# Performance work log

Measured on AMD Instinct MI355X. Metric: run time of the kernel, lower is better.

## Reference

```python
import jax, jax.numpy as jnp
import numpy as np

SCALE_FACTOR = 4.0
DROPOUT_P = 0.5
DROPOUT_KEY = jax.random.key(42)  # fixed key: torch dropout is stochastic; we fix RNG for reproducibility


def setup_inputs() -> dict:
    key = jax.random.key(0)
    k1, k2 = jax.random.split(key)
    x1 = jax.random.normal(k1, (4096, 1024), dtype=jnp.float32)
    x2 = jax.random.normal(k2, (4096, 1024), dtype=jnp.float32)
    return {"x1": x1, "x2": x2}


def reference(x1, x2):
    # scores: [M, N] = x1 @ x2^T, scaled
    scores = jnp.matmul(x1, x2.T) * SCALE_FACTOR
    # F.softmax with no dim on 2-D input -> softmax over dim 1 (keys)
    attn = jax.nn.softmax(scores, axis=-1)
    # dropout p=0.5, train mode (inverted dropout: scale kept units by 1/(1-p))
    keep = jax.random.bernoulli(DROPOUT_KEY, 1.0 - DROPOUT_P, attn.shape)
    attn = jnp.where(keep, attn / (1.0 - DROPOUT_P), 0.0).astype(attn.dtype)
    # output: [M, D] = attn @ x2 (x2 reused as values)
    return jnp.matmul(attn, x2)
```

## Files before the change

### kernel.cpp

```cpp
#include <hip/hip_runtime.h>

typedef unsigned short u16;
typedef unsigned int   u32;
typedef __attribute__((ext_vector_type(4))) float f32x4;
typedef __attribute__((ext_vector_type(8))) short bf16x8;
typedef __attribute__((ext_vector_type(8))) unsigned short u16x8;
typedef __attribute__((ext_vector_type(4))) unsigned short u16x4;

#define MROWS 4096
#define DDIM  1024

__device__ __forceinline__ u16 f2bf(float f) {
  u32 u = __float_as_uint(f);
  return (u16)((u + 0x7FFFu + ((u >> 16) & 1u)) >> 16);
}
__device__ __forceinline__ float bf2f(u16 h) { return __uint_as_float(((u32)h) << 16); }

__device__ __forceinline__ u32 rotl32(u32 x, int r) { return (x << r) | (x >> (32 - r)); }
__device__ __forceinline__ u32 threefry_bits(u32 n) {
  const u32 K0 = 0u, K1 = 42u, K2 = 0x1BD11BDAu ^ 0u ^ 42u;
  u32 x0 = K0;
  u32 x1 = n + K1;
#define TF4(a,b,c,d) \
  x0 += x1; x1 = rotl32(x1, a); x1 ^= x0; \
  x0 += x1; x1 = rotl32(x1, b); x1 ^= x0; \
  x0 += x1; x1 = rotl32(x1, c); x1 ^= x0; \
  x0 += x1; x1 = rotl32(x1, d); x1 ^= x0;
  TF4(13,15,26,6);  x0 += K1; x1 += K2 + 1u;
  TF4(17,29,16,24); x0 += K2; x1 += K0 + 2u;
  TF4(13,15,26,6);  x0 += K0; x1 += K1 + 3u;
  TF4(17,29,16,24); x0 += K1; x1 += K2 + 4u;
  TF4(13,15,26,6);  x0 += K2; x1 += K0 + 5u;
#undef TF4
  return x0 ^ x1;
}

__global__ __launch_bounds__(256)
void expandA(const float4* __restrict__ x, u16* __restrict__ out) {
  int t = blockIdx.x * 256 + threadIdx.x;
  float4 v0 = x[(size_t)t * 2], v1 = x[(size_t)t * 2 + 1];
  float vv[8] = {v0.x*4.f, v0.y*4.f, v0.z*4.f, v0.w*4.f,
                 v1.x*4.f, v1.y*4.f, v1.z*4.f, v1.w*4.f};
  u16 o[24];
#pragma unroll
  for (int j = 0; j < 8; ++j) {
    u16 h = f2bf(vv[j]);
    u16 l = f2bf(vv[j] - bf2f(h));
    o[3*j] = h; o[3*j+1] = h; o[3*j+2] = l;
  }
  u16x8* dst = (u16x8*)(out + (size_t)t * 24);
#pragma unroll
  for (int q = 0; q < 3; ++q) {
    u16x8 wv;
#pragma unroll
    for (int j = 0; j < 8; ++j) wv[j] = o[q*8+j];
    dst[q] = wv;
  }
}

__global__ __launch_bounds__(256)
void castB_transpose(const float* __restrict__ x2, u16* __restrict__ XB,
                     u16* __restrict__ VT) {
  __shared__ float tile[64][65];
  int tid = threadIdx.x;
  int dt = blockIdx.x;
  int kt = blockIdx.y;
#pragma unroll
  for (int it = 0; it < 16; ++it) {
    int lin = it * 256 + tid;
    int r = lin >> 6, c = lin & 63;
    tile[r][c] = x2[(size_t)(kt*64 + r) * DDIM + dt*64 + c];
  }
  __syncthreads();
#pragma unroll
  for (int itr = 0; itr < 2; ++itr) {
    int r  = (tid >> 3) + itr * 32;
    int c0 = (tid & 7) * 8;
    u16 o[24];
#pragma unroll
    for (int j = 0; j < 8; ++j) {
      float v = tile[r][c0 + j];
      u16 h = f2bf(v);
      u16 l = f2bf(v - bf2f(h));
      o[3*j] = h; o[3*j+1] = l; o[3*j+2] = h;
    }
    u16x8* dst = (u16x8*)(XB + (size_t)(kt*64 + r) * 3072 + (size_t)(dt*64 + c0) * 3);
#pragma unroll
    for (int q = 0; q < 3; ++q) {
      u16x8 wv;
#pragma unroll
      for (int j = 0; j < 8; ++j) wv[j] = o[q*8+j];
      dst[q] = wv;
    }
  }
#pragma unroll
  for (int it = 0; it < 16; ++it) {
    int lin = it * 256 + tid;
    int dr = lin >> 6, kc = lin & 63;
    VT[(size_t)(dt*64 + dr) * MROWS + kt*64 + kc] = f2bf(tile[kc][dr]);
  }
}

__device__ __forceinline__ void gload16(const u16* g, u16* l) {
  __builtin_amdgcn_global_load_lds(
      (const __attribute__((address_space(1))) void*)g,
      (__attribute__((address_space(3))) void*)l, 16, 0, 0);
}

#define BARRIER() do { asm volatile("" ::: "memory"); __builtin_amdgcn_s_barrier(); \
                       asm volatile("" ::: "memory"); } while (0)
#define VMCNT(N)  asm volatile("s_waitcnt vmcnt(" #N ")" ::: "memory")
#define PRIO1()   __builtin_amdgcn_s_setprio(1)
#define PRIO0()   __builtin_amdgcn_s_setprio(0)

__device__ __forceinline__ void mma_quad(f32x4 (&acc)[8][4], const bf16x8 (&aF)[4][2],
                                         const bf16x8 (&bF)[2][2], int MH, int NH) {
#pragma unroll
  for (int kx = 0; kx < 2; ++kx)
#pragma unroll
    for (int m = 0; m < 4; ++m)
#pragma unroll
      for (int n = 0; n < 2; ++n)
        acc[MH*4+m][NH*2+n] = __builtin_amdgcn_mfma_f32_16x16x32_bf16(
            aF[m][kx], bF[n][kx], acc[MH*4+m][NH*2+n], 0, 0, 0);
}

template <bool OUT16, bool REMAP>
__global__ __launch_bounds__(512, 2)
void gemm256(const u16* __restrict__ A, const u16* __restrict__ Bt, void* __restrict__ Cv,
             int M, int N, int K, int ntpc) {
  __shared__ u16 smem[65536];
  const int tid = threadIdx.x;
  const int lane = tid & 63;
  const int w = tid >> 6;
  const int wr = w >> 2;
  const int wc = w & 3;
  const int fr = lane & 15;
  const int hi = lane >> 4;

  int bxi, byi;
  if (REMAP) {
    const int id0 = blockIdx.y * gridDim.x + blockIdx.x;
    const int c = id0 & 7, j = id0 >> 3;
    bxi = j >> 1;
    byi = c * 2 + (j & 1);
  } else {
    bxi = blockIdx.x; byi = blockIdx.y;
  }

  const long bm = (long)byi * 256;
  const long bn = (long)bxi * 256;
  const size_t kcol0 = (size_t)blockIdx.z * ntpc * 64;

  const int srow = tid >> 3;
  const int scol = (((tid & 7) ^ (srow & 7)) << 3);
  const u16* Abase = A  + (size_t)(bm + srow) * K + kcol0 + scol;
  const u16* Bbase = Bt + (size_t)(bn + srow) * K + kcol0 + scol;

  const int csw0 = ((hi)     ^ (fr & 7)) << 3;
  const int csw1 = ((4 + hi) ^ (fr & 7)) << 3;
  const int arow = (wr*16 + fr) * 64;
  const int brow = (wc*16 + fr) * 64;

#define RD_A(dst, D, H) do { \
    const u16* _b0 = smem + ((D)*2+(H))*8192 + arow + csw0; \
    const u16* _b1 = smem + ((D)*2+(H))*8192 + arow + csw1; \
    dst[0][0] = *(const bf16x8*)(_b0);        dst[0][1] = *(const bf16x8*)(_b1); \
    dst[1][0] = *(const bf16x8*)(_b0 + 2048); dst[1][1] = *(const bf16x8*)(_b1 + 2048); \
    dst[2][0] = *(const bf16x8*)(_b0 + 4096); dst[2][1] = *(const bf16x8*)(_b1 + 4096); \
    dst[3][0] = *(const bf16x8*)(_b0 + 6144); dst[3][1] = *(const bf16x8*)(_b1 + 6144); } while (0)
#define RD_B(dst, D, H) do { \
    const u16* _b0 = smem + 32768 + ((D)*2+(H))*8192 + brow + csw0; \
    const u16* _b1 = smem + 32768 + ((D)*2+(H))*8192 + brow + csw1; \
    dst[0][0] = *(const bf16x8*)(_b0);        dst[0][1] = *(const bf16x8*)(_b1); \
    dst[1][0] = *(const bf16x8*)(_b0 + 4096); dst[1][1] = *(const bf16x8*)(_b1 + 4096); } while (0)

  f32x4 acc[8][4];
#pragma unroll
  for (int m = 0; m < 8; ++m)
#pragma unroll
    for (int n = 0; n < 4; ++n) acc[m][n] = (f32x4){0.f, 0.f, 0.f, 0.f};
  bf16x8 a0[4][2], a1[4][2], b0[2][2], b1[2][2];

#define STAGE_A(TAU,H,D) do { \
    const u16* _s = Abase + (size_t)(H)*128*K + (size_t)(TAU)*64; \
    u16* _d = smem + ((D)*2+(H))*8192 + tid*8; \
    gload16(_s, _d); gload16(_s + (size_t)64*K, _d + 4096); } while (0)
#define STAGE_B(TAU,H,D) do { \
    const u16* _s = Bbase + (size_t)(H)*128*K + (size_t)(TAU)*64; \
    u16* _d = smem + 32768 + ((D)*2+(H))*8192 + tid*8; \
    gload16(_s, _d); gload16(_s + (size_t)64*K, _d + 4096); } while (0)

  STAGE_A(0,0,0); STAGE_B(0,0,0);
  VMCNT(0); BARRIER();
  RD_A(a0, 0, 0); RD_B(b0, 0, 0);
  STAGE_B(0,1,0);
  STAGE_A(0,1,0);
  STAGE_A(1,0,1); STAGE_B(1,0,1);
  STAGE_B(1,1,1);
  STAGE_A(1,1,1);
  VMCNT(10); BARRIER();

  const int nt = ntpc;
  for (int T = 0; T < nt; T += 2) {
    const int t2 = (T + 2 < nt) ? T + 2 : nt - 1;
    const int t3 = (T + 3 < nt) ? T + 3 : nt - 1;

    RD_B(b1, 0, 1);
    PRIO1(); mma_quad(acc, a0, b0, 0, 0); PRIO0();
    VMCNT(8);  BARRIER();
    RD_A(a1, 0, 1);
    STAGE_A(t2, 0, 0); STAGE_B(t2, 0, 0);
    PRIO1(); mma_quad(acc, a0, b1, 0, 1); PRIO0();
    BARRIER();
    STAGE_B(t2, 1, 0);
    PRIO1(); mma_quad(acc, a1, b0, 1, 0); PRIO0();
    VMCNT(10); BARRIER();
    RD_A(a0, 1, 0); RD_B(b0, 1, 0);
    STAGE_A(t2, 1, 0);
    PRIO1(); mma_quad(acc, a1, b1, 1, 1); PRIO0();
    VMCNT(10); BARRIER();
    RD_B(b1, 1, 1);
    PRIO1(); mma_quad(acc, a0, b0, 0, 0); PRIO0();
    VMCNT(8);  BARRIER();
    RD_A(a1, 1, 1);
    STAGE_A(t3, 0, 1); STAGE_B(t3, 0, 1);
    PRIO1(); mma_quad(acc, a0, b1, 0, 1); PRIO0();
    BARRIER();
    STAGE_B(t3, 1, 1);
    PRIO1(); mma_quad(acc, a1, b0, 1, 0); PRIO0();
    VMCNT(10); BARRIER();
    RD_A(a0, 0, 0); RD_B(b0, 0, 0);
    STAGE_A(t3, 1, 1);
    PRIO1(); mma_quad(acc, a1, b1, 1, 1); PRIO0();
    VMCNT(10); BARRIER();
  }
#undef STAGE_A
#undef STAGE_B
#undef RD_A
#undef RD_B

#pragma unroll
  for (int m = 0; m < 8; ++m)
#pragma unroll
    for (int n = 0; n < 4; ++n) {
      size_t row0 = (size_t)(bm + m*32 + wr*16 + hi*4);
      size_t col  = (size_t)(bn + n*64 + wc*16 + fr);
#pragma unroll
      for (int r = 0; r < 4; ++r) {
        if (OUT16) {
          u16* Cz = (u16*)Cv + (size_t)blockIdx.z * (size_t)M * N;
          Cz[(row0 + r) * N + col] = f2bf(acc[m][n][r]);
        } else {
          float* Cz = (float*)Cv + (size_t)blockIdx.z * (size_t)M * N;
          Cz[(row0 + r) * N + col] = acc[m][n][r];
        }
      }
    }
}

__global__ __launch_bounds__(256)
void softmax_dropout(const float* __restrict__ S, u16* __restrict__ P) {
  const int tid  = threadIdx.x;
  const int lane = tid & 63;
  const int w    = tid >> 6;
  const int row  = blockIdx.x * 4 + w;
  const float4* Sr = (const float4*)(S + (size_t)row * MROWS);
  float4 v[16];
#pragma unroll
  for (int i = 0; i < 16; ++i) v[i] = Sr[i * 64 + lane];
  float m = -3.0e38f;
#pragma unroll
  for (int i = 0; i < 16; ++i)
    m = fmaxf(m, fmaxf(fmaxf(v[i].x, v[i].y), fmaxf(v[i].z, v[i].w)));
#pragma unroll
  for (int off = 32; off > 0; off >>= 1) m = fmaxf(m, __shfl_xor(m, off, 64));
  float s = 0.0f;
#pragma unroll
  for (int i = 0; i < 16; ++i) {
    v[i].x = __expf(v[i].x - m); v[i].y = __expf(v[i].y - m);
    v[i].z = __expf(v[i].z - m); v[i].w = __expf(v[i].w - m);
    s += v[i].x + v[i].y + v[i].z + v[i].w;
  }
#pragma unroll
  for (int off = 32; off > 0; off >>= 1) s += __shfl_xor(s, off, 64);
  const float inv = 2.0f / s;
  u16* Pr = P + (size_t)row * MROWS;
#pragma unroll
  for (int i = 0; i < 16; ++i) {
    int j0 = (i * 64 + lane) * 4;
    u32 base = (u32)row * 4096u + (u32)j0;
    float e[4] = {v[i].x, v[i].y, v[i].z, v[i].w};
    u16x4 o;
#pragma unroll
    for (int c = 0; c < 4; ++c) {
      u32 bits = threefry_bits(base + (u32)c);
      float val = (bits & 0x80000000u) ? 0.0f : e[c] * inv;
      o[c] = f2bf(val);
    }
    *(u16x4*)(Pr + j0) = o;
  }
}

__global__ __launch_bounds__(256)
void reduce4(const u16* __restrict__ p, float4* __restrict__ out) {
  size_t i = (size_t)blockIdx.x * 256 + threadIdx.x;
  const size_t NP = (size_t)MROWS * DDIM;
  u16x4 a = *(const u16x4*)(p + i*4);
  u16x4 b = *(const u16x4*)(p + NP + i*4);
  u16x4 c = *(const u16x4*)(p + 2*NP + i*4);
  u16x4 d = *(const u16x4*)(p + 3*NP + i*4);
  float4 r;
  r.x = bf2f(a[0]) + bf2f(b[0]) + bf2f(c[0]) + bf2f(d[0]);
  r.y = bf2f(a[1]) + bf2f(b[1]) + bf2f(c[1]) + bf2f(d[1]);
  r.z = bf2f(a[2]) + bf2f(b[2]) + bf2f(c[2]) + bf2f(d[2]);
  r.w = bf2f(a[3]) + bf2f(b[3]) + bf2f(c[3]) + bf2f(d[3]);
  out[i] = r;
}

extern "C" void kernel_launch(void* const* d_in, const int* in_sizes, int n_in,
                              void* d_out, int out_size, void* d_ws, size_t ws_size,
                              hipStream_t stream) {
  const float* x1 = (const float*)d_in[0];
  const float* x2 = (const float*)d_in[1];
  float* out = (float*)d_out;
  char* ws = (char*)d_ws;

  const size_t OFF_XB   = 25165824;
  const size_t OFF_VT   = 50331648;
  const size_t OFF_S    = 58720256;
  const size_t NEED     = 125829120;
  if (ws_size < NEED) {
    hipMemsetAsync(d_out, 0x7F, (size_t)out_size * sizeof(float), stream);
    return;
  }
  u16*   XA = (u16*)(ws);
  u16*   XB = (u16*)(ws + OFF_XB);
  u16*   VT = (u16*)(ws + OFF_VT);
  float* S  = (float*)(ws + OFF_S);
  u16*   PT = (u16*)(ws + OFF_S);
  u16*   P  = (u16*)(ws);

  expandA<<<2048, 256, 0, stream>>>((const float4*)x1, XA);
  castB_transpose<<<dim3(16, 64), 256, 0, stream>>>(x2, XB, VT);
  gemm256<false, false><<<dim3(16, 16, 1), 512, 0, stream>>>(XA, XB, S, 4096, 4096, 3072, 48);
  softmax_dropout<<<1024, 256, 0, stream>>>(S, P);
  gemm256<true, true><<<dim3(4, 16, 4), 512, 0, stream>>>(P, VT, PT, 4096, 1024, 4096, 16);
  reduce4<<<4096, 256, 0, stream>>>(PT, (float4*)out);
}
```

Baseline: 187.0 us.

## Split A fragment LDS reads across MMA phases and vectorize V transpose stores

The GEMM main loop now loads each A fragment in two halves spread across successive MMA phases, and the vmcnt waits and barriers are moved to match. The prologue now stages both halves of the first tile before its wait. The aim is to hide LDS read latency behind MFMA work and to reduce stalls at the barriers. The transpose kernel now writes V^T as 16-byte vectors instead of scalar 2-byte stores. The GEMM template is wrapped in two concrete kernels. Moving the waitcnt points risks a race if a staged buffer is read before its global load has landed.

```diff
diff --git a/kernel.cpp b/kernel.cpp
--- a/kernel.cpp
+++ b/kernel.cpp
@@ -94,10 +94,13 @@
     }
   }
 #pragma unroll
-  for (int it = 0; it < 16; ++it) {
-    int lin = it * 256 + tid;
-    int dr = lin >> 6, kc = lin & 63;
-    VT[(size_t)(dt*64 + dr) * MROWS + kt*64 + kc] = f2bf(tile[kc][dr]);
+  for (int it = 0; it < 2; ++it) {
+    int dr  = (tid >> 3) + it * 32;
+    int kc0 = (tid & 7) * 8;
+    u16x8 wv;
+#pragma unroll
+    for (int j = 0; j < 8; ++j) wv[j] = f2bf(tile[kc0 + j][dr]);
+    *(u16x8*)(VT + (size_t)(dt*64 + dr) * MROWS + kt*64 + kc0) = wv;
   }
 }
 
@@ -126,9 +129,10 @@
 }
 
 template <bool OUT16, bool REMAP>
-__global__ __launch_bounds__(512, 2)
-void gemm256(const u16* __restrict__ A, const u16* __restrict__ Bt, void* __restrict__ Cv,
-             int M, int N, int K, int ntpc) {
+__device__ __forceinline__ void gemm_body(const u16* __restrict__ A,
+                                          const u16* __restrict__ Bt,
+                                          void* __restrict__ Cv,
+                                          int M, int N, int K, int ntpc) {
   __shared__ u16 smem[65536];
   const int tid = threadIdx.x;
   const int lane = tid & 63;
@@ -162,18 +166,18 @@
   const int arow = (wr*16 + fr) * 64;
   const int brow = (wc*16 + fr) * 64;
 
-#define RD_A(dst, D, H) do { \
-    const u16* _b0 = smem + ((D)*2+(H))*8192 + arow + csw0; \
-    const u16* _b1 = smem + ((D)*2+(H))*8192 + arow + csw1; \
-    dst[0][0] = *(const bf16x8*)(_b0);        dst[0][1] = *(const bf16x8*)(_b1); \
-    dst[1][0] = *(const bf16x8*)(_b0 + 2048); dst[1][1] = *(const bf16x8*)(_b1 + 2048); \
-    dst[2][0] = *(const bf16x8*)(_b0 + 4096); dst[2][1] = *(const bf16x8*)(_b1 + 4096); \
-    dst[3][0] = *(const bf16x8*)(_b0 + 6144); dst[3][1] = *(const bf16x8*)(_b1 + 6144); } while (0)
+#define RD_A2(dst, D, H, M0) do { \
+    const u16* _p = smem + ((D)*2+(H))*8192 + arow + (M0)*2048; \
+    dst[M0][0]   = *(const bf16x8*)(_p + csw0); \
+    dst[M0][1]   = *(const bf16x8*)(_p + csw1); \
+    dst[M0+1][0] = *(const bf16x8*)(_p + 2048 + csw0); \
+    dst[M0+1][1] = *(const bf16x8*)(_p + 2048 + csw1); } while (0)
 #define RD_B(dst, D, H) do { \
-    const u16* _b0 = smem + 32768 + ((D)*2+(H))*8192 + brow + csw0; \
-    const u16* _b1 = smem + 32768 + ((D)*2+(H))*8192 + brow + csw1; \
-    dst[0][0] = *(const bf16x8*)(_b0);        dst[0][1] = *(const bf16x8*)(_b1); \
-    dst[1][0] = *(const bf16x8*)(_b0 + 4096); dst[1][1] = *(const bf16x8*)(_b1 + 4096); } while (0)
+    const u16* _p = smem + 32768 + ((D)*2+(H))*8192 + brow; \
+    dst[0][0] = *(const bf16x8*)(_p + csw0); \
+    dst[0][1] = *(const bf16x8*)(_p + csw1); \
+    dst[1][0] = *(const bf16x8*)(_p + 4096 + csw0); \
+    dst[1][1] = *(const bf16x8*)(_p + 4096 + csw1); } while (0)
 
   f32x4 acc[8][4];
 #pragma unroll
@@ -192,52 +196,53 @@
     gload16(_s, _d); gload16(_s + (size_t)64*K, _d + 4096); } while (0)
 
   STAGE_A(0,0,0); STAGE_B(0,0,0);
+  STAGE_B(0,1,0); STAGE_A(0,1,0);
   VMCNT(0); BARRIER();
-  RD_A(a0, 0, 0); RD_B(b0, 0, 0);
-  STAGE_B(0,1,0);
-  STAGE_A(0,1,0);
+  RD_A2(a0,0,0,0); RD_A2(a0,0,0,2); RD_B(b0,0,0);
   STAGE_A(1,0,1); STAGE_B(1,0,1);
   STAGE_B(1,1,1);
   STAGE_A(1,1,1);
-  VMCNT(10); BARRIER();
+  BARRIER();
 
   const int nt = ntpc;
   for (int T = 0; T < nt; T += 2) {
     const int t2 = (T + 2 < nt) ? T + 2 : nt - 1;
     const int t3 = (T + 3 < nt) ? T + 3 : nt - 1;
 
-    RD_B(b1, 0, 1);
+    RD_B(b1, 0, 1); RD_A2(a1, 0, 1, 0);
     PRIO1(); mma_quad(acc, a0, b0, 0, 0); PRIO0();
-    VMCNT(8);  BARRIER();
-    RD_A(a1, 0, 1);
+    BARRIER();
+    RD_A2(a1, 0, 1, 2);
     STAGE_A(t2, 0, 0); STAGE_B(t2, 0, 0);
     PRIO1(); mma_quad(acc, a0, b1, 0, 1); PRIO0();
-    BARRIER();
+    VMCNT(10); BARRIER();
+    RD_A2(a0, 1, 0, 0);
     STAGE_B(t2, 1, 0);
     PRIO1(); mma_quad(acc, a1, b0, 1, 0); PRIO0();
     VMCNT(10); BARRIER();
-    RD_A(a0, 1, 0); RD_B(b0, 1, 0);
+    RD_A2(a0, 1, 0, 2); RD_B(b0, 1, 0);
     STAGE_A(t2, 1, 0);
     PRIO1(); mma_quad(acc, a1, b1, 1, 1); PRIO0();
-    VMCNT(10); BARRIER();
-    RD_B(b1, 1, 1);
+    VMCNT(8); BARRIER();
+    RD_B(b1, 1, 1); RD_A2(a1, 1, 1, 0);
     PRIO1(); mma_quad(acc, a0, b0, 0, 0); PRIO0();
-    VMCNT(8);  BARRIER();
-    RD_A(a1, 1, 1);
+    BARRIER();
+    RD_A2(a1, 1, 1, 2);
     STAGE_A(t3, 0, 1); STAGE_B(t3, 0, 1);
     PRIO1(); mma_quad(acc, a0, b1, 0, 1); PRIO0();
-    BARRIER();
+    VMCNT(10); BARRIER();
+    RD_A2(a0, 0, 0, 0);
     STAGE_B(t3, 1, 1);
     PRIO1(); mma_quad(acc, a1, b0, 1, 0); PRIO0();
     VMCNT(10); BARRIER();
-    RD_A(a0, 0, 0); RD_B(b0, 0, 0);
+    RD_A2(a0, 0, 0, 2); RD_B(b0, 0, 0);
     STAGE_A(t3, 1, 1);
     PRIO1(); mma_quad(acc, a1, b1, 1, 1); PRIO0();
-    VMCNT(10); BARRIER();
+    VMCNT(8); BARRIER();
   }
 #undef STAGE_A
 #undef STAGE_B
-#undef RD_A
+#undef RD_A2
 #undef RD_B
 
 #pragma unroll
@@ -257,6 +262,17 @@
         }
       }
     }
+}
+
+__global__ __launch_bounds__(512, 2)
+void gemm_qk(const u16* __restrict__ A, const u16* __restrict__ Bt,
+             void* __restrict__ Cv, int M, int N, int K, int ntpc) {
+  gemm_body<false, false>(A, Bt, Cv, M, N, K, ntpc);
+}
+__global__ __launch_bounds__(512, 2)
+void gemm_pv(const u16* __restrict__ A, const u16* __restrict__ Bt,
+             void* __restrict__ Cv, int M, int N, int K, int ntpc) {
+  gemm_body<true, true>(A, Bt, Cv, M, N, K, ntpc);
 }
 
 __global__ __launch_bounds__(256)
@@ -343,8 +359,8 @@
 
   expandA<<<2048, 256, 0, stream>>>((const float4*)x1, XA);
   castB_transpose<<<dim3(16, 64), 256, 0, stream>>>(x2, XB, VT);
-  gemm256<false, false><<<dim3(16, 16, 1), 512, 0, stream>>>(XA, XB, S, 4096, 4096, 3072, 48);
+  gemm_qk<<<dim3(16, 16, 1), 512, 0, stream>>>(XA, XB, S, 4096, 4096, 3072, 48);
   softmax_dropout<<<1024, 256, 0, stream>>>(S, P);
-  gemm256<true, true><<<dim3(4, 16, 4), 512, 0, stream>>>(P, VT, PT, 4096, 1024, 4096, 16);
+  gemm_pv<<<dim3(4, 16, 4), 512, 0, stream>>>(P, VT, PT, 4096, 1024, 4096, 16);
   reduce4<<<4096, 256, 0, stream>>>(PT, (float4*)out);
 }
```

Measured after the change: 186.4 us. No clear change (-0.4%).
